# Kernel tuning notes

Hardware: AMD Instinct MI355X
Metric: run time of the kernel (lower is better)

## Reference

```python
import jax, jax.numpy as jnp
import numpy as np

N_NODES = 100000


def setup_inputs() -> dict:
    key = jax.random.key(0)
    k_x, k_e, k_w1, k_b1, k_w2, k_b2 = jax.random.split(key, 6)
    num_features, hidden, num_classes = 128, 64, 32
    x = jax.random.normal(k_x, (N_NODES, num_features), dtype=jnp.float32)
    edge_index = jax.random.randint(k_e, (2, 1600000), 0, N_NODES, dtype=jnp.int64)
    # torch.nn.Linear default init: U(-1/sqrt(fan_in), 1/sqrt(fan_in))
    s1 = 1.0 / np.sqrt(num_features)
    s2 = 1.0 / np.sqrt(hidden)
    W1 = jax.random.uniform(k_w1, (num_features, hidden), jnp.float32, -s1, s1)
    b1 = jax.random.uniform(k_b1, (hidden,), jnp.float32, -s1, s1)
    W2 = jax.random.uniform(k_w2, (hidden, num_classes), jnp.float32, -s2, s2)
    b2 = jax.random.uniform(k_b2, (num_classes,), jnp.float32, -s2, s2)
    return {"x": x, "edge_index": edge_index, "W1": W1, "b1": b1, "W2": W2, "b2": b2}


def reference(x, edge_index, W1, b1, W2, b2):
    # GNNConv: linear then scatter-add aggregation with self-loops
    xl = x @ W1 + b1                      # [N, hidden]
    src, dst = edge_index[0], edge_index[1]
    msgs = xl[src]                        # gather source features [E, hidden]
    agg = jax.ops.segment_sum(msgs, dst, num_segments=N_NODES)
    agg = agg + xl                        # add_self_loops contributes xl to each node
    h = jax.nn.relu(agg)
    return h @ W2 + b2                    # [N, num_classes]
```

## Files before the change

### kernel.cpp

```cpp
#include <hip/hip_runtime.h>
#include <hip/hip_bf16.h>

#define TPB 256
#define BSHIFT 7
#define BNODES (1 << BSHIFT)
#define NWRITERS 256

typedef int vint4 __attribute__((ext_vector_type(4)));
typedef __attribute__((ext_vector_type(8))) short short8v;
typedef __attribute__((ext_vector_type(4))) float f32x4;

__device__ __forceinline__ unsigned short f2bf(float f) {
    unsigned int u = __float_as_uint(f);
    u += 0x7fffu + ((u >> 16) & 1u);
    return (unsigned short)(u >> 16);
}
__device__ __forceinline__ float bflo(unsigned int u) { return __uint_as_float(u << 16); }
__device__ __forceinline__ float bfhi(unsigned int u) { return __uint_as_float(u & 0xffff0000u); }

__global__ __launch_bounds__(TPB) void k_gemm1_hist(
    const float* __restrict__ x, const float* __restrict__ W1, const float* __restrict__ b1,
    unsigned int* __restrict__ xlb,
    const int* __restrict__ ei, int* __restrict__ cntT,
    int N, int E, int NB, int CH)
{
    __shared__ unsigned short wT[64 * 136];
    __shared__ float b1s[64];
    __shared__ int   lcnt[1024];

    const int t = threadIdx.x;

    if ((int)blockIdx.x < NWRITERS) {
        const int hb = blockIdx.x;
        const int start = hb * CH;
        const int lim = min(E, start + CH);
        for (int j = t; j < NB; j += TPB) lcnt[j] = 0;
        __syncthreads();
        const int* dst = ei + E;
        int i = start + t * 4;
        for (; i + 3 < lim; i += TPB * 4) {
            vint4 d = __builtin_nontemporal_load(reinterpret_cast<const vint4*>(dst + i));
            atomicAdd(&lcnt[d.x >> BSHIFT], 1);
            atomicAdd(&lcnt[d.y >> BSHIFT], 1);
            atomicAdd(&lcnt[d.z >> BSHIFT], 1);
            atomicAdd(&lcnt[d.w >> BSHIFT], 1);
        }
        for (i = start + ((lim - start) & ~3) + t; i < lim; i += TPB)
            atomicAdd(&lcnt[dst[i] >> BSHIFT], 1);
        __syncthreads();
        for (int j = t; j < NB; j += TPB) cntT[j * NWRITERS + hb] = lcnt[j];
        return;
    }

    for (int i = t; i < 2048; i += TPB) {
        int k = i >> 4, cw = (i & 15) * 4;
        float4 u = reinterpret_cast<const float4*>(W1)[i];
        wT[(cw + 0) * 136 + k] = f2bf(u.x);
        wT[(cw + 1) * 136 + k] = f2bf(u.y);
        wT[(cw + 2) * 136 + k] = f2bf(u.z);
        wT[(cw + 3) * 136 + k] = f2bf(u.w);
    }
    if (t < 64) b1s[t] = b1[t];
    __syncthreads();

    const int l = t & 63, wid = t >> 6;
    const int cl = l & 15, kg = l >> 4;
    const int rw = ((int)blockIdx.x - NWRITERS) * 64 + wid * 16;
    if (rw >= N) return;
    const int r = rw + cl;

    const float4* xp4 = reinterpret_cast<const float4*>(x) + ((size_t)min(r, N - 1) * 32 + kg * 2);

    f32x4 acc[4] = {};
    #pragma unroll
    for (int kt = 0; kt < 4; ++kt) {
        float4 fA = xp4[kt * 8];
        float4 fB = xp4[kt * 8 + 1];
        short8v a;
        a[0] = (short)f2bf(fA.x); a[1] = (short)f2bf(fA.y);
        a[2] = (short)f2bf(fA.z); a[3] = (short)f2bf(fA.w);
        a[4] = (short)f2bf(fB.x); a[5] = (short)f2bf(fB.y);
        a[6] = (short)f2bf(fB.z); a[7] = (short)f2bf(fB.w);
        #pragma unroll
        for (int ct = 0; ct < 4; ++ct) {
            short8v b = *reinterpret_cast<const short8v*>(
                &wT[(ct * 16 + cl) * 136 + kt * 32 + kg * 8]);
            acc[ct] = __builtin_amdgcn_mfma_f32_16x16x32_bf16(a, b, acc[ct], 0, 0, 0);
        }
    }

    #pragma unroll
    for (int ct = 0; ct < 4; ++ct) {
        #pragma unroll
        for (int reg = 0; reg < 4; ++reg) {
            int row = rw + kg * 4 + reg;
            float v = acc[ct][reg] + b1s[ct * 16 + cl];
            unsigned int m = (unsigned int)f2bf(v);
            unsigned int p = (unsigned int)__shfl_xor((int)m, 1);
            if (!(l & 1) && row < N)
                xlb[(size_t)row * 32 + ct * 8 + (cl >> 1)] = m | (p << 16);
        }
    }
}

__global__ __launch_bounds__(TPB) void k_colscan(
    const int* __restrict__ cntT, int* __restrict__ segT, int* __restrict__ totals, int NB)
{
    __shared__ int wsum[4];
    const int r = blockIdx.x;
    const int t = threadIdx.x;
    const int lane = t & 63, wid = t >> 6;
    int v = cntT[r * NWRITERS + t];
    int incl = v;
    for (int d = 1; d < 64; d <<= 1) {
        int n = __shfl_up(incl, d);
        if (lane >= d) incl += n;
    }
    if (lane == 63) wsum[wid] = incl;
    __syncthreads();
    int woff = 0;
    for (int w = 0; w < wid; w++) woff += wsum[w];
    int excl = woff + incl - v;
    segT[r * NWRITERS + t] = excl;
    if (t == TPB - 1) totals[r] = excl + v;
}

__global__ __launch_bounds__(TPB) void k_fillbin(
    const int* __restrict__ ei, const int* __restrict__ segT, const int* __restrict__ totals,
    unsigned int* __restrict__ recs, int E, int NB, int CH)
{
    __shared__ int lcur[1024];
    __shared__ int bbs[1024];
    __shared__ int wsum[4];
    const int blk = blockIdx.x;
    const int t = threadIdx.x;
    const int lane = t & 63, wid = t >> 6;

    const int b4 = t * 4;
    int v0 = (b4 + 0 < NB) ? totals[b4 + 0] : 0;
    int v1 = (b4 + 1 < NB) ? totals[b4 + 1] : 0;
    int v2 = (b4 + 2 < NB) ? totals[b4 + 2] : 0;
    int v3 = (b4 + 3 < NB) ? totals[b4 + 3] : 0;
    int tsum = v0 + v1 + v2 + v3;
    int incl = tsum;
    for (int d = 1; d < 64; d <<= 1) {
        int n = __shfl_up(incl, d);
        if (lane >= d) incl += n;
    }
    if (lane == 63) wsum[wid] = incl;
    __syncthreads();
    int woff = 0;
    for (int w = 0; w < wid; w++) woff += wsum[w];
    int texcl = woff + incl - tsum;
    if (b4 + 0 < NB) bbs[b4 + 0] = texcl;
    if (b4 + 1 < NB) bbs[b4 + 1] = texcl + v0;
    if (b4 + 2 < NB) bbs[b4 + 2] = texcl + v0 + v1;
    if (b4 + 3 < NB) bbs[b4 + 3] = texcl + v0 + v1 + v2;
    __syncthreads();

    for (int j = t; j < NB; j += TPB)
        lcur[j] = bbs[j] + segT[j * NWRITERS + blk];
    __syncthreads();

    const int start = blk * CH;
    const int lim = min(E, start + CH);
    const int* src = ei;
    const int* dst = ei + E;
    int i = start + t * 4;
    for (; i + 3 < lim; i += TPB * 4) {
        vint4 d = __builtin_nontemporal_load(reinterpret_cast<const vint4*>(dst + i));
        vint4 s = __builtin_nontemporal_load(reinterpret_cast<const vint4*>(src + i));
        int p0 = atomicAdd(&lcur[d.x >> BSHIFT], 1);
        int p1 = atomicAdd(&lcur[d.y >> BSHIFT], 1);
        int p2 = atomicAdd(&lcur[d.z >> BSHIFT], 1);
        int p3 = atomicAdd(&lcur[d.w >> BSHIFT], 1);
        recs[p0] = ((unsigned int)s.x << BSHIFT) | (unsigned int)(d.x & (BNODES-1));
        recs[p1] = ((unsigned int)s.y << BSHIFT) | (unsigned int)(d.y & (BNODES-1));
        recs[p2] = ((unsigned int)s.z << BSHIFT) | (unsigned int)(d.z & (BNODES-1));
        recs[p3] = ((unsigned int)s.w << BSHIFT) | (unsigned int)(d.w & (BNODES-1));
    }
    for (i = start + ((lim - start) & ~3) + t; i < lim; i += TPB) {
        int d = dst[i];
        int p = atomicAdd(&lcur[d >> BSHIFT], 1);
        recs[p] = ((unsigned int)src[i] << BSHIFT) | (unsigned int)(d & (BNODES-1));
    }
}

__global__ __launch_bounds__(TPB) void k_bsort(
    const unsigned int* __restrict__ recs, const int* __restrict__ totals,
    int* __restrict__ esrc, int* __restrict__ off, int N, int NB, int E)
{
    __shared__ int h[BNODES];
    __shared__ int cur[BNODES];
    __shared__ int ws2[2];
    __shared__ int red[4];

    const int r = blockIdx.x;
    const int t = threadIdx.x;
    const int lane = t & 63, w = t >> 6;

    int s = 0;
    for (int j = t; j < r; j += TPB) s += totals[j];
    #pragma unroll
    for (int d = 32; d >= 1; d >>= 1) s += __shfl_xor(s, d);
    if (lane == 0) red[w] = s;
    if (t < BNODES) h[t] = 0;
    __syncthreads();
    const int bb0 = red[0] + red[1] + red[2] + red[3];
    const int bb1 = bb0 + totals[r];

    for (int i = bb0 + t; i < bb1; i += TPB)
        atomicAdd(&h[recs[i] & (BNODES - 1)], 1);
    __syncthreads();

    int v = 0, incl = 0;
    if (t < BNODES) {
        v = h[t];
        incl = v;
        for (int d = 1; d < 64; d <<= 1) {
            int n = __shfl_up(incl, d);
            if (lane >= d) incl += n;
        }
        if (lane == 63) ws2[w] = incl;
    }
    __syncthreads();
    if (t < BNODES) {
        int excl = incl - v + (w ? ws2[0] : 0);
        cur[t] = bb0 + excl;
        int node = r * BNODES + t;
        if (node < N) off[node] = bb0 + excl;
    }
    if (r == NB - 1 && t == 0) off[N] = E;
    __syncthreads();

    for (int i = bb0 + t; i < bb1; i += TPB) {
        unsigned int rec = recs[i];
        int p = atomicAdd(&cur[rec & (BNODES - 1)], 1);
        esrc[p] = (int)(rec >> BSHIFT);
    }
}

#define AGG_BLOCKS 12288
__global__ __launch_bounds__(TPB) void k_agg(
    const unsigned int* __restrict__ xlb,
    const int* __restrict__ off,
    const int* __restrict__ esrc,
    const float* __restrict__ W2,
    const float* __restrict__ b2,
    float* __restrict__ out, int N)
{
    __shared__ float w2s[64 * 32];
    __shared__ float b2s[32];
    __shared__ float arow[4][68];

    const int t = threadIdx.x;
    const float4* w4 = reinterpret_cast<const float4*>(W2);
    for (int i = t; i < 512; i += TPB) {
        float4 u = w4[i];
        int o = i * 4;
        w2s[o+0] = u.x; w2s[o+1] = u.y; w2s[o+2] = u.z; w2s[o+3] = u.w;
    }
    if (t < 32) b2s[t] = b2[t];
    __syncthreads();

    const int wid = t >> 6, lane = t & 63;
    const int slot = lane >> 3, b = lane & 7;
    const int c = lane & 31, h = lane >> 5;
    const uint4* xb4 = reinterpret_cast<const uint4*>(xlb);

    for (int node = blockIdx.x * 4 + wid; node < N; node += gridDim.x * 4) {
        const int beg = off[node], end = off[node + 1];
        float a0=0.f,a1=0.f,a2=0.f,a3=0.f,a4=0.f,a5=0.f,a6=0.f,a7=0.f;
        int e = beg + slot;
        for (; e + 8 < end; e += 16) {
            int s0 = __builtin_nontemporal_load(esrc + e);
            int s1 = __builtin_nontemporal_load(esrc + e + 8);
            uint4 v0 = xb4[(size_t)s0 * 8 + b];
            uint4 v1 = xb4[(size_t)s1 * 8 + b];
            a0 += bflo(v0.x); a1 += bfhi(v0.x);
            a2 += bflo(v0.y); a3 += bfhi(v0.y);
            a4 += bflo(v0.z); a5 += bfhi(v0.z);
            a6 += bflo(v0.w); a7 += bfhi(v0.w);
            a0 += bflo(v1.x); a1 += bfhi(v1.x);
            a2 += bflo(v1.y); a3 += bfhi(v1.y);
            a4 += bflo(v1.z); a5 += bfhi(v1.z);
            a6 += bflo(v1.w); a7 += bfhi(v1.w);
        }
        if (e < end) {
            int s = __builtin_nontemporal_load(esrc + e);
            uint4 v = xb4[(size_t)s * 8 + b];
            a0 += bflo(v.x); a1 += bfhi(v.x);
            a2 += bflo(v.y); a3 += bfhi(v.y);
            a4 += bflo(v.z); a5 += bfhi(v.z);
            a6 += bflo(v.w); a7 += bfhi(v.w);
        }
        #pragma unroll
        for (int d = 8; d <= 32; d <<= 1) {
            a0 += __shfl_xor(a0, d); a1 += __shfl_xor(a1, d);
            a2 += __shfl_xor(a2, d); a3 += __shfl_xor(a3, d);
            a4 += __shfl_xor(a4, d); a5 += __shfl_xor(a5, d);
            a6 += __shfl_xor(a6, d); a7 += __shfl_xor(a7, d);
        }
        if (slot == 0) {
            uint4 sv = xb4[(size_t)node * 8 + b];
            float* p = &arow[wid][b * 8];
            p[0] = fmaxf(a0 + bflo(sv.x), 0.f);
            p[1] = fmaxf(a1 + bfhi(sv.x), 0.f);
            p[2] = fmaxf(a2 + bflo(sv.y), 0.f);
            p[3] = fmaxf(a3 + bfhi(sv.y), 0.f);
            p[4] = fmaxf(a4 + bflo(sv.z), 0.f);
            p[5] = fmaxf(a5 + bfhi(sv.z), 0.f);
            p[6] = fmaxf(a6 + bflo(sv.w), 0.f);
            p[7] = fmaxf(a7 + bfhi(sv.w), 0.f);
        }
        float o = 0.f;
        const float* ar = &arow[wid][h * 32];
        const float* wp = &w2s[h * 32 * 32 + c];
        #pragma unroll
        for (int kk = 0; kk < 32; kk++)
            o = fmaf(ar[kk], wp[kk * 32], o);
        o += __shfl_xor(o, 32);
        if (h == 0)
            __builtin_nontemporal_store(o + b2s[c], out + (size_t)node * 32 + c);
    }
}

extern "C" void kernel_launch(void* const* d_in, const int* in_sizes, int n_in,
                              void* d_out, int out_size, void* d_ws, size_t ws_size,
                              hipStream_t stream) {
    const float* x  = (const float*)d_in[0];
    const int*   ei = (const int*)d_in[1];
    const float* W1 = (const float*)d_in[2];
    const float* b1 = (const float*)d_in[3];
    const float* W2 = (const float*)d_in[4];
    const float* b2 = (const float*)d_in[5];
    float* out = (float*)d_out;

    const int N = in_sizes[0] / 128;
    const int E = in_sizes[1] / 2;
    const int NB = (N + BNODES - 1) >> BSHIFT;
    const int CH = (((E + NWRITERS - 1) / NWRITERS) + 3) & ~3;

    char* w = (char*)d_ws;
    unsigned int* xlb = (unsigned int*)w;   w += (size_t)N * 32 * 4;
    int* cntT   = (int*)w;                  w += (size_t)NB * NWRITERS * 4;
    int* segT   = (int*)w;                  w += (size_t)NB * NWRITERS * 4;
    int* totals = (int*)w;                  w += ((size_t)NB * 4 + 15) & ~15ull;
    int* off    = (int*)w;                  w += ((size_t)(N + 1) * 4 + 15) & ~15ull;
    unsigned int* recs = (unsigned int*)w;  w += (size_t)E * 4;
    int* esrc   = (int*)w;

    const int nbG = (N + 63) / 64;

    hipLaunchKernelGGL(k_gemm1_hist, dim3(NWRITERS + nbG), dim3(TPB), 0, stream,
                       x, W1, b1, xlb, ei, cntT, N, E, NB, CH);
    hipLaunchKernelGGL(k_colscan, dim3(NB), dim3(TPB), 0, stream, cntT, segT, totals, NB);
    hipLaunchKernelGGL(k_fillbin, dim3(NWRITERS), dim3(TPB), 0, stream,
                       ei, segT, totals, recs, E, NB, CH);
    hipLaunchKernelGGL(k_bsort, dim3(NB), dim3(TPB), 0, stream,
                       recs, totals, esrc, off, N, NB, E);
    hipLaunchKernelGGL(k_agg, dim3(AGG_BLOCKS), dim3(TPB), 0, stream,
                       xlb, off, esrc, W2, b2, out, N);
}
```

Measured before the change: 132.9 us.

## Split aggregation into feature-quarter gather kernel and separate tiled GEMM2 kernel

The fused gather+GEMM2 kernel is split in two. The first kernel aggregates neighbors for one quarter of the 64 features per block, using 8-byte loads so each block touches a narrower slice of xl, which should improve cache locality. It writes ReLU'd bf16 aggregates to a new workspace buffer. A second kernel then runs the 64x32 GEMM over 64-row tiles held in shared memory. This adds an extra kernel launch, an intermediate round trip through memory, and rounds the aggregate to bf16 before the GEMM, and it reads the edge list four times.

```diff
diff --git a/kernel.cpp b/kernel.cpp
--- a/kernel.cpp
+++ b/kernel.cpp
@@ -240,20 +240,72 @@
     }
 }
 
-#define AGG_BLOCKS 12288
-__global__ __launch_bounds__(TPB) void k_agg(
+#define AGGQ_BLOCKS 8192
+__global__ __launch_bounds__(TPB) void k_aggq(
     const unsigned int* __restrict__ xlb,
     const int* __restrict__ off,
     const int* __restrict__ esrc,
+    unsigned int* __restrict__ aggb,
+    int N)
+{
+    const int t = threadIdx.x;
+    const int wid = t >> 6, lane = t & 63;
+    const int sl = lane >> 2, fl = lane & 3;
+    const int q = blockIdx.x & 3;
+    const int qidx = blockIdx.x >> 2;
+    const int qstride = (gridDim.x >> 2) * 4;
+    const uint2* xb2 = reinterpret_cast<const uint2*>(xlb);
+    uint2* ab2 = reinterpret_cast<uint2*>(aggb);
+
+    for (int node = qidx * 4 + wid; node < N; node += qstride) {
+        const int beg = off[node], end = off[node + 1];
+        float a0 = 0.f, a1 = 0.f, a2 = 0.f, a3 = 0.f;
+        int e = beg + sl;
+        for (; e + 16 < end; e += 32) {
+            int s0 = esrc[e];
+            int s1 = esrc[e + 16];
+            uint2 v0 = xb2[(size_t)s0 * 16 + q * 4 + fl];
+            uint2 v1 = xb2[(size_t)s1 * 16 + q * 4 + fl];
+            a0 += bflo(v0.x); a1 += bfhi(v0.x); a2 += bflo(v0.y); a3 += bfhi(v0.y);
+            a0 += bflo(v1.x); a1 += bfhi(v1.x); a2 += bflo(v1.y); a3 += bfhi(v1.y);
+        }
+        if (e < end) {
+            uint2 v = xb2[(size_t)esrc[e] * 16 + q * 4 + fl];
+            a0 += bflo(v.x); a1 += bfhi(v.x); a2 += bflo(v.y); a3 += bfhi(v.y);
+        }
+        #pragma unroll
+        for (int d = 4; d <= 32; d <<= 1) {
+            a0 += __shfl_xor(a0, d); a1 += __shfl_xor(a1, d);
+            a2 += __shfl_xor(a2, d); a3 += __shfl_xor(a3, d);
+        }
+        if (sl == 0) {
+            uint2 sv = xb2[(size_t)node * 16 + q * 4 + fl];
+            float r0 = fmaxf(a0 + bflo(sv.x), 0.f);
+            float r1 = fmaxf(a1 + bfhi(sv.x), 0.f);
+            float r2 = fmaxf(a2 + bflo(sv.y), 0.f);
+            float r3 = fmaxf(a3 + bfhi(sv.y), 0.f);
+            uint2 pk;
+            pk.x = (unsigned int)f2bf(r0) | ((unsigned int)f2bf(r1) << 16);
+            pk.y = (unsigned int)f2bf(r2) | ((unsigned int)f2bf(r3) << 16);
+            ab2[(size_t)node * 16 + q * 4 + fl] = pk;
+        }
+    }
+}
+
+__global__ __launch_bounds__(TPB) void k_gemm2b(
+    const unsigned int* __restrict__ aggb,
     const float* __restrict__ W2,
     const float* __restrict__ b2,
     float* __restrict__ out, int N)
 {
     __shared__ float w2s[64 * 32];
+    __shared__ float as[64 * 68];
     __shared__ float b2s[32];
-    __shared__ float arow[4][68];
-
-    const int t = threadIdx.x;
+
+    const int t = threadIdx.x;
+    const int rbase = blockIdx.x * 64;
+    const int rows = min(64, N - rbase);
+
     const float4* w4 = reinterpret_cast<const float4*>(W2);
     for (int i = t; i < 512; i += TPB) {
         float4 u = w4[i];
@@ -261,67 +313,35 @@
         w2s[o+0] = u.x; w2s[o+1] = u.y; w2s[o+2] = u.z; w2s[o+3] = u.w;
     }
     if (t < 32) b2s[t] = b2[t];
-    __syncthreads();
-
-    const int wid = t >> 6, lane = t & 63;
-    const int slot = lane >> 3, b = lane & 7;
-    const int c = lane & 31, h = lane >> 5;
-    const uint4* xb4 = reinterpret_cast<const uint4*>(xlb);
-
-    for (int node = blockIdx.x * 4 + wid; node < N; node += gridDim.x * 4) {
-        const int beg = off[node], end = off[node + 1];
-        float a0=0.f,a1=0.f,a2=0.f,a3=0.f,a4=0.f,a5=0.f,a6=0.f,a7=0.f;
-        int e = beg + slot;
-        for (; e + 8 < end; e += 16) {
-            int s0 = __builtin_nontemporal_load(esrc + e);
-            int s1 = __builtin_nontemporal_load(esrc + e + 8);
-            uint4 v0 = xb4[(size_t)s0 * 8 + b];
-            uint4 v1 = xb4[(size_t)s1 * 8 + b];
-            a0 += bflo(v0.x); a1 += bfhi(v0.x);
-            a2 += bflo(v0.y); a3 += bfhi(v0.y);
-            a4 += bflo(v0.z); a5 += bfhi(v0.z);
-            a6 += bflo(v0.w); a7 += bfhi(v0.w);
-            a0 += bflo(v1.x); a1 += bfhi(v1.x);
-            a2 += bflo(v1.y); a3 += bfhi(v1.y);
-            a4 += bflo(v1.z); a5 += bfhi(v1.z);
-            a6 += bflo(v1.w); a7 += bfhi(v1.w);
-        }
-        if (e < end) {
-            int s = __builtin_nontemporal_load(esrc + e);
-            uint4 v = xb4[(size_t)s * 8 + b];
-            a0 += bflo(v.x); a1 += bfhi(v.x);
-            a2 += bflo(v.y); a3 += bfhi(v.y);
-            a4 += bflo(v.z); a5 += bfhi(v.z);
-            a6 += bflo(v.w); a7 += bfhi(v.w);
-        }
+
+    const uint4* a4 = reinterpret_cast<const uint4*>(aggb + (size_t)rbase * 32);
+    for (int i = t; i < rows * 8; i += TPB) {
+        uint4 v = a4[i];
+        int row = i >> 3, kk = (i & 7) * 8;
+        float* p = &as[row * 68 + kk];
+        p[0] = bflo(v.x); p[1] = bfhi(v.x);
+        p[2] = bflo(v.y); p[3] = bfhi(v.y);
+        p[4] = bflo(v.z); p[5] = bfhi(v.z);
+        p[6] = bflo(v.w); p[7] = bfhi(v.w);
+    }
+    __syncthreads();
+
+    const int row = t >> 2, cg = t & 3;
+    if (row < rows) {
+        float acc[8];
         #pragma unroll
-        for (int d = 8; d <= 32; d <<= 1) {
-            a0 += __shfl_xor(a0, d); a1 += __shfl_xor(a1, d);
-            a2 += __shfl_xor(a2, d); a3 += __shfl_xor(a3, d);
-            a4 += __shfl_xor(a4, d); a5 += __shfl_xor(a5, d);
-            a6 += __shfl_xor(a6, d); a7 += __shfl_xor(a7, d);
-        }
-        if (slot == 0) {
-            uint4 sv = xb4[(size_t)node * 8 + b];
-            float* p = &arow[wid][b * 8];
-            p[0] = fmaxf(a0 + bflo(sv.x), 0.f);
-            p[1] = fmaxf(a1 + bfhi(sv.x), 0.f);
-            p[2] = fmaxf(a2 + bflo(sv.y), 0.f);
-            p[3] = fmaxf(a3 + bfhi(sv.y), 0.f);
-            p[4] = fmaxf(a4 + bflo(sv.z), 0.f);
-            p[5] = fmaxf(a5 + bfhi(sv.z), 0.f);
-            p[6] = fmaxf(a6 + bflo(sv.w), 0.f);
-            p[7] = fmaxf(a7 + bfhi(sv.w), 0.f);
-        }
-        float o = 0.f;
-        const float* ar = &arow[wid][h * 32];
-        const float* wp = &w2s[h * 32 * 32 + c];
-        #pragma unroll
-        for (int kk = 0; kk < 32; kk++)
-            o = fmaf(ar[kk], wp[kk * 32], o);
-        o += __shfl_xor(o, 32);
-        if (h == 0)
-            __builtin_nontemporal_store(o + b2s[c], out + (size_t)node * 32 + c);
+        for (int c = 0; c < 8; c++) acc[c] = b2s[cg*8 + c];
+        const float* ar = &as[row * 68];
+        #pragma unroll 4
+        for (int k = 0; k < 64; k++) {
+            float a = ar[k];
+            const float* wp = &w2s[k*32 + cg*8];
+            #pragma unroll
+            for (int c = 0; c < 8; c++) acc[c] = fmaf(a, wp[c], acc[c]);
+        }
+        float4* op = reinterpret_cast<float4*>(out + (size_t)(rbase + row) * 32 + cg * 8);
+        op[0] = make_float4(acc[0], acc[1], acc[2], acc[3]);
+        op[1] = make_float4(acc[4], acc[5], acc[6], acc[7]);
     }
 }
 
@@ -342,7 +362,8 @@
     const int CH = (((E + NWRITERS - 1) / NWRITERS) + 3) & ~3;
 
     char* w = (char*)d_ws;
-    unsigned int* xlb = (unsigned int*)w;   w += (size_t)N * 32 * 4;
+    unsigned int* xlb  = (unsigned int*)w;  w += (size_t)N * 32 * 4;
+    unsigned int* aggb = (unsigned int*)w;  w += (size_t)N * 32 * 4;
     int* cntT   = (int*)w;                  w += (size_t)NB * NWRITERS * 4;
     int* segT   = (int*)w;                  w += (size_t)NB * NWRITERS * 4;
     int* totals = (int*)w;                  w += ((size_t)NB * 4 + 15) & ~15ull;
@@ -359,6 +380,8 @@
                        ei, segT, totals, recs, E, NB, CH);
     hipLaunchKernelGGL(k_bsort, dim3(NB), dim3(TPB), 0, stream,
                        recs, totals, esrc, off, N, NB, E);
-    hipLaunchKernelGGL(k_agg, dim3(AGG_BLOCKS), dim3(TPB), 0, stream,
-                       xlb, off, esrc, W2, b2, out, N);
-}
+    hipLaunchKernelGGL(k_aggq, dim3(AGGQ_BLOCKS), dim3(TPB), 0, stream,
+                       xlb, off, esrc, aggb, N);
+    hipLaunchKernelGGL(k_gemm2b, dim3(nbG), dim3(TPB), 0, stream,
+                       aggb, W2, b2, out, N);
+}
```

Result: slower. 194.1 us (+46.0%).
